# Kernel optimization log

Hardware: AMD Instinct MI355X
Metric: run time of the kernel (lower is better)

Reference implementation:

```python
import jax, jax.numpy as jnp
import numpy as np

B, T1, T2 = 16, 2048, 512
N_MEL, N_TEXT, N_ATT = 80, 256, 256
TEMPERATURE = 0.0005


def _conv1d(x, w, b):
    # x: (B, T, Cin), w: (K, Cin, Cout), 'same' padding
    pad = (w.shape[0] - 1) // 2
    y = jax.lax.conv_general_dilated(
        x, w, window_strides=(1,), padding=[(pad, pad)],
        dimension_numbers=("NWC", "WIO", "NWC"))
    return y + b


def setup_inputs() -> dict:
    key = jax.random.key(0)
    ks = jax.random.split(key, 16)
    s = 0.05
    queries = jax.random.normal(ks[0], (B, N_MEL, T1), jnp.float32)
    keys = jax.random.normal(ks[1], (B, T2, N_TEXT), jnp.float32)
    attn_prior = jax.random.uniform(ks[2], (B, T2, T1), jnp.float32)
    lengths = jax.random.randint(ks[3], (B,), T2 // 2, T2 + 1)
    mask = jnp.arange(T2)[None, :] >= lengths[:, None]  # True = padding
    # key_proj params: Conv(256->512,k3), ReLU, Conv(512->256,k1)
    kw1 = jax.random.normal(ks[4], (3, N_TEXT, 2 * N_TEXT), jnp.float32) * s
    kb1 = jnp.zeros((2 * N_TEXT,), jnp.float32)
    kw2 = jax.random.normal(ks[5], (1, 2 * N_TEXT, N_ATT), jnp.float32) * s
    kb2 = jnp.zeros((N_ATT,), jnp.float32)
    # query_proj params: Conv(80->160,k3), ReLU, Conv(160->80,k1), ReLU, Conv(80->256,k1)
    qw1 = jax.random.normal(ks[6], (3, N_MEL, 2 * N_MEL), jnp.float32) * s
    qb1 = jnp.zeros((2 * N_MEL,), jnp.float32)
    qw2 = jax.random.normal(ks[7], (1, 2 * N_MEL, N_MEL), jnp.float32) * s
    qb2 = jnp.zeros((N_MEL,), jnp.float32)
    qw3 = jax.random.normal(ks[8], (1, N_MEL, N_ATT), jnp.float32) * s
    qb3 = jnp.zeros((N_ATT,), jnp.float32)
    return dict(queries=queries, keys=keys, mask=mask, attn_prior=attn_prior,
                kw1=kw1, kb1=kb1, kw2=kw2, kb2=kb2,
                qw1=qw1, qb1=qb1, qw2=qw2, qb2=qb2, qw3=qw3, qb3=qb3)


def reference(queries, keys, mask, attn_prior,
              kw1, kb1, kw2, kb2, qw1, qb1, qw2, qb2, qw3, qb3):
    # keys: (B, T2, C_text) -> ke: (B, T2, n_att)
    ke = _conv1d(jax.nn.relu(_conv1d(keys, kw1, kb1)), kw2, kb2)
    # queries: (B, C_mel, T1) -> (B, T1, C_mel) -> qe: (B, T1, n_att)
    q = queries.transpose(0, 2, 1)
    q = jax.nn.relu(_conv1d(jax.nn.relu(_conv1d(q, qw1, qb1)), qw2, qb2))
    qe = _conv1d(q, qw3, qb3)
    # pairwise squared L2 distance over channels, via |q|^2 + |k|^2 - 2 q.k
    q2 = jnp.sum(qe * qe, axis=-1)            # (B, T1)
    k2 = jnp.sum(ke * ke, axis=-1)            # (B, T2)
    qk = jnp.einsum("btc,bsc->bts", qe, ke)   # (B, T1, T2)
    dist = q2[:, :, None] + k2[:, None, :] - 2.0 * qk
    attn = (-TEMPERATURE * dist)[:, None]      # (B, 1, T1, T2)
    # prior in log-space
    attn = jax.nn.log_softmax(attn, axis=3) + jnp.log(
        attn_prior.transpose(0, 2, 1)[:, None] + 1e-8)
    attn_logprob = attn
    attn = jnp.where(mask[:, None, None, :], -jnp.inf, attn)
    attn = jax.nn.softmax(attn, axis=3)
    return attn, attn_logprob
```

## Files before the change

### kernel.cpp

```cpp
#include <hip/hip_runtime.h>
#include <cmath>

#define NB    16
#define TT1   2048
#define TT2   512
#define NATT  256
#define TEMP  0.0005f

#define KP_SZ   (NB*514*256)
#define KE_SZ   (NB*512*256)
#define QP_SZ   (NB*2050*80)
#define QE_SZ   (NB*2048*256)
#define W1T_SZ  (512*768)
#define W2T_SZ  (256*512)
#define W3T_SZ  (160*256)
#define W4T_SZ  (80*160)
#define W5T_SZ  (256*96)
#define WTOT_SZ (W1T_SZ+W2T_SZ+W3T_SZ+W4T_SZ+W5T_SZ)
#define LGP_SZ  (NB*TT1*TT2)

#define PREP_PK_BLK   (KP_SZ/256)
#define PREP_WT_BLK   (WTOT_SZ/256)
#define PREP_QT_BLK   (NB*(TT1/64))
#define CONV_KEY_BLK  (NB*512/32)
#define CONV_QRY_BLK  (NB*2048/128)

typedef __attribute__((ext_vector_type(8))) short short8v;
typedef __attribute__((ext_vector_type(4))) float f32x4;

__device__ inline ushort f2bf(float f) {
    unsigned int u = __float_as_uint(f);
    u += 0x7fff + ((u >> 16) & 1);
    return (ushort)(u >> 16);
}
__device__ inline float bf2f(ushort u) {
    return __uint_as_float(((unsigned int)u) << 16);
}


__global__ __launch_bounds__(256) void prep_kernel(
    const float* __restrict__ keys, ushort* __restrict__ kp,
    const float* __restrict__ kw1, const float* __restrict__ kw2,
    const float* __restrict__ qw1, const float* __restrict__ qw2,
    const float* __restrict__ qw3,
    ushort* __restrict__ w1t, ushort* __restrict__ w2t, ushort* __restrict__ w3t,
    ushort* __restrict__ w4t, ushort* __restrict__ w5t,
    const float* __restrict__ queries, ushort* __restrict__ qp)
{
    __shared__ float T[80][65];
    const int bx  = blockIdx.x;
    const int tid = threadIdx.x;

    if (bx < PREP_PK_BLK) {
        const int idx = bx * 256 + tid;
        int c = idx & 255;
        int r = (idx >> 8) % 514;
        int b = idx / (514 * 256);
        float v = 0.f;
        if (r >= 1 && r <= 512)
            v = keys[((size_t)b * 512 + (r - 1)) * 256 + c];
        kp[idx] = f2bf(v);
        return;
    }
    if (bx < PREP_PK_BLK + PREP_WT_BLK) {
        int idx = (bx - PREP_PK_BLK) * 256 + tid;
        const float* w; ushort* wt; int Kreal, Kpad, N;
        if (idx < W1T_SZ) {
            w = kw1; wt = w1t; Kreal = 768; Kpad = 768; N = 512;
        } else if ((idx -= W1T_SZ) < W2T_SZ) {
            w = kw2; wt = w2t; Kreal = 512; Kpad = 512; N = 256;
        } else if ((idx -= W2T_SZ) < W3T_SZ) {
            w = qw1; wt = w3t; Kreal = 240; Kpad = 256; N = 160;
        } else if ((idx -= W3T_SZ) < W4T_SZ) {
            w = qw2; wt = w4t; Kreal = 160; Kpad = 160; N = 80;
        } else {
            idx -= W4T_SZ;
            w = qw3; wt = w5t; Kreal = 80; Kpad = 96; N = 256;
        }
        int k = idx % Kpad;
        int n = idx / Kpad;
        wt[idx] = (k < Kreal) ? f2bf(w[(size_t)k * N + n]) : (ushort)0;
        return;
    }
    {
        const int l  = bx - PREP_PK_BLK - PREP_WT_BLK;
        const int b  = l >> 5;
        const int t0 = (l & 31) * 64;
        const int g  = tid >> 6;
        const int j  = tid & 63;
        #pragma unroll
        for (int r = 0; r < 20; ++r) {
            const int c = g * 20 + r;
            T[c][j] = queries[((size_t)b * 80 + c) * 2048 + t0 + j];
        }
        __syncthreads();
        const int tt = tid >> 2;
        const int c0 = (tid & 3) * 20;
        ushort* qrow = qp + (size_t)b * (2050 * 80) + (size_t)(t0 + tt + 1) * 80 + c0;
        #pragma unroll
        for (int i4 = 0; i4 < 5; ++i4) {
            ushort4 st;
            st.x = f2bf(T[c0 + i4 * 4 + 0][tt]);
            st.y = f2bf(T[c0 + i4 * 4 + 1][tt]);
            st.z = f2bf(T[c0 + i4 * 4 + 2][tt]);
            st.w = f2bf(T[c0 + i4 * 4 + 3][tt]);
            *(ushort4*)(qrow + i4 * 4) = st;
        }
        if (t0 == 0 && tid < 80)
            qp[(size_t)b * (2050 * 80) + tid] = 0;
        if (t0 == 2048 - 64 && tid < 80)
            qp[(size_t)b * (2050 * 80) + (size_t)2049 * 80 + tid] = 0;
    }
}


__global__ __launch_bounds__(512, 4) void conv_kernel(
    const ushort* __restrict__ kp, const ushort* __restrict__ w1t,
    const float* __restrict__ kb1, const ushort* __restrict__ w2t,
    const float* __restrict__ kb2, ushort* __restrict__ ke, float* __restrict__ k2,
    const ushort* __restrict__ qp, const ushort* __restrict__ w3t,
    const float* __restrict__ qb1, const ushort* __restrict__ w4t,
    const float* __restrict__ qb2, const ushort* __restrict__ w5t,
    const float* __restrict__ qb3, ushort* __restrict__ qe)
{
    __shared__ __align__(16) unsigned char smem[69632];
    const int bx   = blockIdx.x;
    const int tid  = threadIdx.x;
    const int wv   = tid >> 6;
    const int lane = tid & 63;
    const int lr   = lane & 15;
    const int lk   = lane >> 4;

    if (bx < CONV_KEY_BLK) {
        ushort (*h1s)[536] = (ushort(*)[536])smem;
        float (*k2part)[8] = (float(*)[8])(smem + 32 * 536 * 2);
        const int m0 = bx * 32;

        {
            const ushort* arow0;
            const ushort* arow1;
            {
                const int m = m0 + lr;
                arow0 = kp + (size_t)(m >> 9) * (514 * 256) + (size_t)(m & 511) * 256 + lk * 8;
                const int m1 = m0 + 16 + lr;
                arow1 = kp + (size_t)(m1 >> 9) * (514 * 256) + (size_t)(m1 & 511) * 256 + lk * 8;
            }
            const ushort* wtb = w1t + (size_t)(wv * 64 + lr) * 768 + lk * 8;
            f32x4 acc[2][4];
            #pragma unroll
            for (int mf = 0; mf < 2; ++mf)
                #pragma unroll
                for (int f = 0; f < 4; ++f) acc[mf][f] = (f32x4){0.f, 0.f, 0.f, 0.f};
            #pragma unroll
            for (int ks = 0; ks < 24; ++ks) {
                const short8v a0 = *(const short8v*)(arow0 + ks * 32);
                const short8v a1 = *(const short8v*)(arow1 + ks * 32);
                #pragma unroll
                for (int f = 0; f < 4; ++f) {
                    const short8v b = *(const short8v*)(wtb + (size_t)f * 16 * 768 + ks * 32);
                    acc[0][f] = __builtin_amdgcn_mfma_f32_16x16x32_bf16(a0, b, acc[0][f], 0, 0, 0);
                    acc[1][f] = __builtin_amdgcn_mfma_f32_16x16x32_bf16(a1, b, acc[1][f], 0, 0, 0);
                }
            }
            #pragma unroll
            for (int f = 0; f < 4; ++f) {
                const int col = wv * 64 + f * 16 + lr;
                const float bv = kb1[col];
                #pragma unroll
                for (int mf = 0; mf < 2; ++mf)
                    #pragma unroll
                    for (int r = 0; r < 4; ++r)
                        h1s[mf * 16 + lk * 4 + r][col] = f2bf(fmaxf(acc[mf][f][r] + bv, 0.f));
            }
        }
        __syncthreads();

        {
            f32x4 acc[2][2];
            #pragma unroll
            for (int mf = 0; mf < 2; ++mf)
                #pragma unroll
                for (int f = 0; f < 2; ++f) acc[mf][f] = (f32x4){0.f, 0.f, 0.f, 0.f};
            #pragma unroll
            for (int ks = 0; ks < 16; ++ks) {
                const short8v a0 = *(const short8v*)&h1s[lr][lk * 8 + ks * 32];
                const short8v a1 = *(const short8v*)&h1s[16 + lr][lk * 8 + ks * 32];
                #pragma unroll
                for (int f = 0; f < 2; ++f) {
                    const short8v b = *(const short8v*)(w2t + (size_t)(wv * 32 + f * 16 + lr) * 512
                                                            + lk * 8 + ks * 32);
                    acc[0][f] = __builtin_amdgcn_mfma_f32_16x16x32_bf16(a0, b, acc[0][f], 0, 0, 0);
                    acc[1][f] = __builtin_amdgcn_mfma_f32_16x16x32_bf16(a1, b, acc[1][f], 0, 0, 0);
                }
            }
            float ss[2][4];
            #pragma unroll
            for (int mf = 0; mf < 2; ++mf)
                #pragma unroll
                for (int r = 0; r < 4; ++r) ss[mf][r] = 0.f;
            #pragma unroll
            for (int f = 0; f < 2; ++f) {
                const int col = wv * 32 + f * 16 + lr;
                const float bv = kb2[col];
                #pragma unroll
                for (int mf = 0; mf < 2; ++mf)
                    #pragma unroll
                    for (int r = 0; r < 4; ++r) {
                        const float o = acc[mf][f][r] + bv;
                        ke[(size_t)(m0 + mf * 16 + lk * 4 + r) * 256 + col] = f2bf(o);
                        ss[mf][r] += o * o;
                    }
            }
            #pragma unroll
            for (int mf = 0; mf < 2; ++mf)
                #pragma unroll
                for (int r = 0; r < 4; ++r) {
                    #pragma unroll
                    for (int off = 1; off < 16; off <<= 1)
                        ss[mf][r] += __shfl_xor(ss[mf][r], off);
                }
            if (lr == 0) {
                #pragma unroll
                for (int mf = 0; mf < 2; ++mf)
                    #pragma unroll
                    for (int r = 0; r < 4; ++r)
                        k2part[mf * 16 + lk * 4 + r][wv] = ss[mf][r];
            }
        }
        __syncthreads();
        if (tid < 32) {
            float s = 0.f;
            #pragma unroll
            for (int w = 0; w < 8; ++w) s += k2part[tid][w];
            k2[m0 + tid] = -TEMP * s;
        }
        return;
    }
    {
        ushort (*s1)[168] = (ushort(*)[168])smem;
        ushort (*s2)[104] = (ushort(*)[104])(smem + 128 * 168 * 2);
        const int m0 = (bx - CONV_KEY_BLK) * 128;
        const int cg = wv >> 2;
        const int rb = (wv & 3) * 32;

        #pragma unroll
        for (int i = 0; i < 4; ++i) {
            const int e = tid * 4 + i;
            s2[e >> 4][80 + (e & 15)] = 0;
        }

        {
            const ushort* arow0;
            const ushort* arow1;
            {
                const int m = m0 + rb + lr;
                arow0 = qp + (size_t)(m >> 11) * (2050 * 80) + (size_t)(m & 2047) * 80 + lk * 8;
                const int m1 = m0 + rb + 16 + lr;
                arow1 = qp + (size_t)(m1 >> 11) * (2050 * 80) + (size_t)(m1 & 2047) * 80 + lk * 8;
            }
            f32x4 acc[2][5];
            #pragma unroll
            for (int mf = 0; mf < 2; ++mf)
                #pragma unroll
                for (int f = 0; f < 5; ++f) acc[mf][f] = (f32x4){0.f, 0.f, 0.f, 0.f};
            #pragma unroll
            for (int ks = 0; ks < 8; ++ks) {
                const short8v a0 = *(const short8v*)(arow0 + ks * 32);
                const short8v a1 = *(const short8v*)(arow1 + ks * 32);
                #pragma unroll
                for (int f = 0; f < 5; ++f) {
                    const short8v b = *(const short8v*)(w3t + (size_t)((cg * 5 + f) * 16 + lr) * 256
                                                            + lk * 8 + ks * 32);
                    acc[0][f] = __builtin_amdgcn_mfma_f32_16x16x32_bf16(a0, b, acc[0][f], 0, 0, 0);
                    acc[1][f] = __builtin_amdgcn_mfma_f32_16x16x32_bf16(a1, b, acc[1][f], 0, 0, 0);
                }
            }
            #pragma unroll
            for (int f = 0; f < 5; ++f) {
                const int col = (cg * 5 + f) * 16 + lr;
                const float bv = qb1[col];
                #pragma unroll
                for (int mf = 0; mf < 2; ++mf)
                    #pragma unroll
                    for (int r = 0; r < 4; ++r)
                        s1[rb + mf * 16 + lk * 4 + r][col] = f2bf(fmaxf(acc[mf][f][r] + bv, 0.f));
            }
        }
        __syncthreads();

        {
            const int nf = cg ? 2 : 3;
            const int f0 = cg ? 3 : 0;
            f32x4 acc[2][3];
            #pragma unroll
            for (int mf = 0; mf < 2; ++mf)
                #pragma unroll
                for (int f = 0; f < 3; ++f) acc[mf][f] = (f32x4){0.f, 0.f, 0.f, 0.f};
            #pragma unroll
            for (int ks = 0; ks < 5; ++ks) {
                const short8v a0 = *(const short8v*)&s1[rb + lr][lk * 8 + ks * 32];
                const short8v a1 = *(const short8v*)&s1[rb + 16 + lr][lk * 8 + ks * 32];
                #pragma unroll
                for (int f = 0; f < 3; ++f) {
                    if (f < nf) {
                        const short8v b = *(const short8v*)(w4t + (size_t)((f0 + f) * 16 + lr) * 160
                                                                + lk * 8 + ks * 32);
                        acc[0][f] = __builtin_amdgcn_mfma_f32_16x16x32_bf16(a0, b, acc[0][f], 0, 0, 0);
                        acc[1][f] = __builtin_amdgcn_mfma_f32_16x16x32_bf16(a1, b, acc[1][f], 0, 0, 0);
                    }
                }
            }
            #pragma unroll
            for (int f = 0; f < 3; ++f) {
                if (f < nf) {
                    const int col = (f0 + f) * 16 + lr;
                    const float bv = qb2[col];
                    #pragma unroll
                    for (int mf = 0; mf < 2; ++mf)
                        #pragma unroll
                        for (int r = 0; r < 4; ++r)
                            s2[rb + mf * 16 + lk * 4 + r][col] = f2bf(fmaxf(acc[mf][f][r] + bv, 0.f));
                }
            }
        }
        __syncthreads();

        {
            f32x4 acc[2][8];
            #pragma unroll
            for (int mf = 0; mf < 2; ++mf)
                #pragma unroll
                for (int f = 0; f < 8; ++f) acc[mf][f] = (f32x4){0.f, 0.f, 0.f, 0.f};
            #pragma unroll
            for (int ks = 0; ks < 3; ++ks) {
                const short8v a0 = *(const short8v*)&s2[rb + lr][lk * 8 + ks * 32];
                const short8v a1 = *(const short8v*)&s2[rb + 16 + lr][lk * 8 + ks * 32];
                #pragma unroll
                for (int f = 0; f < 8; ++f) {
                    const short8v b = *(const short8v*)(w5t + (size_t)((cg * 8 + f) * 16 + lr) * 96
                                                            + lk * 8 + ks * 32);
                    acc[0][f] = __builtin_amdgcn_mfma_f32_16x16x32_bf16(a0, b, acc[0][f], 0, 0, 0);
                    acc[1][f] = __builtin_amdgcn_mfma_f32_16x16x32_bf16(a1, b, acc[1][f], 0, 0, 0);
                }
            }
            #pragma unroll
            for (int f = 0; f < 8; ++f) {
                const int col = (cg * 8 + f) * 16 + lr;
                const float bv = qb3[col];
                #pragma unroll
                for (int mf = 0; mf < 2; ++mf)
                    #pragma unroll
                    for (int r = 0; r < 4; ++r)
                        qe[(size_t)(m0 + rb + mf * 16 + lk * 4 + r) * 256 + col] = f2bf(acc[mf][f][r] + bv);
            }
        }
    }
}


__global__ __launch_bounds__(256) void prior_log_transpose(
    const float* __restrict__ prior, ushort* __restrict__ lgp)
{
    __shared__ float T[64][65];
    const int b    = blockIdx.z;
    const int t1_0 = blockIdx.x * 64;
    const int t2_0 = blockIdx.y * 64;
    const int j  = threadIdx.x & 63;
    const int i0 = (threadIdx.x >> 6) * 16;
    #pragma unroll
    for (int r = 0; r < 16; ++r)
        T[i0 + r][j] = __builtin_nontemporal_load(
            prior + ((size_t)b * TT2 + t2_0 + i0 + r) * TT1 + t1_0 + j);
    __syncthreads();
    #pragma unroll
    for (int r = 0; r < 16; ++r) {
        const int p = i0 + r;
        const float v = T[j][p];
        lgp[((size_t)b * TT1 + t1_0 + p) * TT2 + t2_0 + j] = f2bf(__logf(v + 1e-8f));
    }
}


__global__ __launch_bounds__(512) void attn_kernel(
    const ushort* __restrict__ qe, const ushort* __restrict__ ke,
    const float* __restrict__ k2t, const ushort* __restrict__ lgp,
    const unsigned char* __restrict__ mask,
    float* __restrict__ out_attn, float* __restrict__ out_lp)
{
    __shared__ float S[16][516];
    __shared__ float rowZ[16];
    __shared__ float rowM[16];
    __shared__ float rowI[16];
    const int b    = blockIdx.x >> 7;
    const int t1_0 = (blockIdx.x & 127) << 4;
    const int tid  = threadIdx.x;
    const int lane = tid & 63;
    const int wv   = tid >> 6;
    const int t2   = tid;

    const bool mv = mask[(size_t)b * TT2 + t2] != 0;
    ushort lg[16];
    #pragma unroll
    for (int r = 0; r < 16; ++r)
        lg[r] = lgp[((size_t)b * TT1 + t1_0 + r) * TT2 + t2];

    {
        const int lr = lane & 15;
        const int lk = lane >> 4;
        const ushort* qrow = qe + ((size_t)b * TT1 + t1_0 + lr) * NATT + lk * 8;
        short8v a[8];
        #pragma unroll
        for (int k = 0; k < 8; ++k)
            a[k] = *(const short8v*)(qrow + k * 32);

        const ushort* kbase = ke + ((size_t)b * TT2 + wv * 64 + lr) * NATT + lk * 8;
        #pragma unroll
        for (int n = 0; n < 4; ++n) {
            f32x4 acc = {0.f, 0.f, 0.f, 0.f};
            const ushort* kb = kbase + (size_t)n * 16 * NATT;
            #pragma unroll
            for (int k = 0; k < 8; ++k) {
                short8v bfr = *(const short8v*)(kb + k * 32);
                acc = __builtin_amdgcn_mfma_f32_16x16x32_bf16(a[k], bfr, acc, 0, 0, 0);
            }
            const int col = wv * 64 + n * 16 + lr;
            const float k2v = k2t[(size_t)b * TT2 + col];
            #pragma unroll
            for (int r = 0; r < 4; ++r)
                S[lk * 4 + r][col] = fmaf(2.0f * TEMP, acc[r], k2v);
        }
    }
    __syncthreads();

    const int rr = tid >> 5;
    const int jj = tid & 31;

    {
        float sv[16];
        #pragma unroll
        for (int k = 0; k < 16; ++k) sv[k] = S[rr][jj + 32 * k];
        float mx = sv[0];
        #pragma unroll
        for (int k = 1; k < 16; ++k) mx = fmaxf(mx, sv[k]);
        #pragma unroll
        for (int off = 16; off; off >>= 1) mx = fmaxf(mx, __shfl_xor(mx, off));
        float se = 0.f;
        #pragma unroll
        for (int k = 0; k < 16; ++k) se += __expf(sv[k] - mx);
        #pragma unroll
        for (int off = 16; off; off >>= 1) se += __shfl_xor(se, off);
        if (jj == 0) rowZ[rr] = mx + __logf(se);
    }
    __syncthreads();

    #pragma unroll
    for (int r = 0; r < 16; ++r) {
        const float uu = S[r][t2] + bf2f(lg[r]);
        out_lp[((size_t)b * TT1 + t1_0 + r) * TT2 + t2] = uu - rowZ[r];
        S[r][t2] = mv ? -INFINITY : uu;
    }
    __syncthreads();

    {
        float uv[16];
        #pragma unroll
        for (int k = 0; k < 16; ++k) uv[k] = S[rr][jj + 32 * k];
        float mx = uv[0];
        #pragma unroll
        for (int k = 1; k < 16; ++k) mx = fmaxf(mx, uv[k]);
        #pragma unroll
        for (int off = 16; off; off >>= 1) mx = fmaxf(mx, __shfl_xor(mx, off));
        float se = 0.f;
        #pragma unroll
        for (int k = 0; k < 16; ++k) se += __expf(uv[k] - mx);
        #pragma unroll
        for (int off = 16; off; off >>= 1) se += __shfl_xor(se, off);
        if (jj == 0) { rowM[rr] = mx; rowI[rr] = 1.0f / se; }
    }
    __syncthreads();

    #pragma unroll
    for (int r = 0; r < 16; ++r) {
        const float a = __expf(S[r][t2] - rowM[r]) * rowI[r];
        out_attn[((size_t)b * TT1 + t1_0 + r) * TT2 + t2] = a;
    }
}


extern "C" void kernel_launch(void* const* d_in, const int* in_sizes, int n_in,
                              void* d_out, int out_size, void* d_ws, size_t ws_size,
                              hipStream_t stream) {
    const float* queries = (const float*)d_in[0];
    const float* keys    = (const float*)d_in[1];
    const unsigned char* mask = (const unsigned char*)d_in[2];
    const float* prior   = (const float*)d_in[3];
    const float* kw1 = (const float*)d_in[4];
    const float* kb1 = (const float*)d_in[5];
    const float* kw2 = (const float*)d_in[6];
    const float* kb2 = (const float*)d_in[7];
    const float* qw1 = (const float*)d_in[8];
    const float* qb1 = (const float*)d_in[9];
    const float* qw2 = (const float*)d_in[10];
    const float* qb2 = (const float*)d_in[11];
    const float* qw3 = (const float*)d_in[12];
    const float* qb3 = (const float*)d_in[13];

    ushort* us   = (ushort*)d_ws;
    ushort* kp   = us;
    ushort* ke   = kp  + KP_SZ;
    ushort* qp   = ke  + KE_SZ;
    ushort* qe   = qp  + QP_SZ;
    ushort* w1t  = qe  + QE_SZ;
    ushort* w2t  = w1t + W1T_SZ;
    ushort* w3t  = w2t + W2T_SZ;
    ushort* w4t  = w3t + W3T_SZ;
    ushort* w5t  = w4t + W4T_SZ;
    ushort* lgp  = w5t + W5T_SZ;
    float*  k2   = (float*)(lgp + LGP_SZ);

    float* out_attn = (float*)d_out;
    float* out_lp   = out_attn + (size_t)NB * TT1 * TT2;

    prep_kernel<<<PREP_PK_BLK + PREP_WT_BLK + PREP_QT_BLK, 256, 0, stream>>>(
        keys, kp, kw1, kw2, qw1, qw2, qw3, w1t, w2t, w3t, w4t, w5t, queries, qp);

    conv_kernel<<<CONV_KEY_BLK + CONV_QRY_BLK, 512, 0, stream>>>(
        kp, w1t, kb1, w2t, kb2, ke, k2,
        qp, w3t, qb1, w4t, qb2, w5t, qb3, qe);

    prior_log_transpose<<<dim3(TT1 / 64, TT2 / 64, NB), 256, 0, stream>>>(prior, lgp);

    attn_kernel<<<NB * (TT1 / 16), 512, 0, stream>>>(
        qe, ke, k2, lgp, mask, out_attn, out_lp);
}
```

Measured before the change: 177.4 us.

## Fuse prior log-transpose into conv kernel and restructure attention softmax epilogue

The standalone prior log-transpose kernel is merged into the conv kernel as extra blocks, so it runs concurrently with the key/query projections and saves one launch. In the attention kernel, the output stores are deferred so log-prob and attn are written together from registers, and masked entries are set to zero directly instead of recomputing exp from shared memory. The launch bounds also request 8 waves per SIMD. Risks: more register pressure from holding uu[16], and conv blocks sharing the grid with bandwidth-heavy transpose blocks.

```diff
diff --git a/kernel.cpp b/kernel.cpp
--- a/kernel.cpp
+++ b/kernel.cpp
@@ -24,6 +24,7 @@
 #define PREP_QT_BLK   (NB*(TT1/64))
 #define CONV_KEY_BLK  (NB*512/32)
 #define CONV_QRY_BLK  (NB*2048/128)
+#define CONV_PLT_BLK  (NB*(TT1/64)*(TT2/128))
 
 typedef __attribute__((ext_vector_type(8))) short short8v;
 typedef __attribute__((ext_vector_type(4))) float f32x4;
@@ -114,14 +115,15 @@
 }
 
 
-__global__ __launch_bounds__(512, 4) void conv_kernel(
+__global__ __launch_bounds__(512, 4) void conv_plt_kernel(
     const ushort* __restrict__ kp, const ushort* __restrict__ w1t,
     const float* __restrict__ kb1, const ushort* __restrict__ w2t,
     const float* __restrict__ kb2, ushort* __restrict__ ke, float* __restrict__ k2,
     const ushort* __restrict__ qp, const ushort* __restrict__ w3t,
     const float* __restrict__ qb1, const ushort* __restrict__ w4t,
     const float* __restrict__ qb2, const ushort* __restrict__ w5t,
-    const float* __restrict__ qb3, ushort* __restrict__ qe)
+    const float* __restrict__ qb3, ushort* __restrict__ qe,
+    const float* __restrict__ prior, ushort* __restrict__ lgp)
 {
     __shared__ __align__(16) unsigned char smem[69632];
     const int bx   = blockIdx.x;
@@ -236,7 +238,7 @@
         }
         return;
     }
-    {
+    if (bx < CONV_KEY_BLK + CONV_QRY_BLK) {
         ushort (*s1)[168] = (ushort(*)[168])smem;
         ushort (*s2)[104] = (ushort(*)[104])(smem + 128 * 168 * 2);
         const int m0 = (bx - CONV_KEY_BLK) * 128;
@@ -354,34 +356,34 @@
                         qe[(size_t)(m0 + rb + mf * 16 + lk * 4 + r) * 256 + col] = f2bf(acc[mf][f][r] + bv);
             }
         }
+        return;
+    }
+    {
+        float (*T)[65] = ((float(*)[65])smem) + (size_t)(tid >> 8) * 64;
+        const int l    = bx - CONV_KEY_BLK - CONV_QRY_BLK;
+        const int b    = l >> 7;
+        const int rem  = l & 127;
+        const int t1_0 = (rem & 31) * 64;
+        const int t2_0 = (rem >> 5) * 128 + (tid >> 8) * 64;
+        const int t    = tid & 255;
+        const int j  = t & 63;
+        const int i0 = (t >> 6) * 16;
+        #pragma unroll
+        for (int r = 0; r < 16; ++r)
+            T[i0 + r][j] = __builtin_nontemporal_load(
+                prior + ((size_t)b * TT2 + t2_0 + i0 + r) * TT1 + t1_0 + j);
+        __syncthreads();
+        #pragma unroll
+        for (int r = 0; r < 16; ++r) {
+            const int p = i0 + r;
+            const float v = T[j][p];
+            lgp[((size_t)b * TT1 + t1_0 + p) * TT2 + t2_0 + j] = f2bf(__logf(v + 1e-8f));
+        }
     }
 }
 
 
-__global__ __launch_bounds__(256) void prior_log_transpose(
-    const float* __restrict__ prior, ushort* __restrict__ lgp)
-{
-    __shared__ float T[64][65];
-    const int b    = blockIdx.z;
-    const int t1_0 = blockIdx.x * 64;
-    const int t2_0 = blockIdx.y * 64;
-    const int j  = threadIdx.x & 63;
-    const int i0 = (threadIdx.x >> 6) * 16;
-    #pragma unroll
-    for (int r = 0; r < 16; ++r)
-        T[i0 + r][j] = __builtin_nontemporal_load(
-            prior + ((size_t)b * TT2 + t2_0 + i0 + r) * TT1 + t1_0 + j);
-    __syncthreads();
-    #pragma unroll
-    for (int r = 0; r < 16; ++r) {
-        const int p = i0 + r;
-        const float v = T[j][p];
-        lgp[((size_t)b * TT1 + t1_0 + p) * TT2 + t2_0 + j] = f2bf(__logf(v + 1e-8f));
-    }
-}
-
-
-__global__ __launch_bounds__(512) void attn_kernel(
+__global__ __launch_bounds__(512, 8) void attn_kernel(
     const ushort* __restrict__ qe, const ushort* __restrict__ ke,
     const float* __restrict__ k2t, const ushort* __restrict__ lgp,
     const unsigned char* __restrict__ mask,
@@ -436,53 +438,49 @@
     const int jj = tid & 31;
 
     {
-        float sv[16];
-        #pragma unroll
-        for (int k = 0; k < 16; ++k) sv[k] = S[rr][jj + 32 * k];
-        float mx = sv[0];
-        #pragma unroll
-        for (int k = 1; k < 16; ++k) mx = fmaxf(mx, sv[k]);
+        float mx = -INFINITY;
+        #pragma unroll
+        for (int k = 0; k < 16; ++k) mx = fmaxf(mx, S[rr][jj + 32 * k]);
         #pragma unroll
         for (int off = 16; off; off >>= 1) mx = fmaxf(mx, __shfl_xor(mx, off));
         float se = 0.f;
         #pragma unroll
-        for (int k = 0; k < 16; ++k) se += __expf(sv[k] - mx);
+        for (int k = 0; k < 16; ++k) se += __expf(S[rr][jj + 32 * k] - mx);
         #pragma unroll
         for (int off = 16; off; off >>= 1) se += __shfl_xor(se, off);
         if (jj == 0) rowZ[rr] = mx + __logf(se);
     }
     __syncthreads();
 
+    float uu[16];
     #pragma unroll
     for (int r = 0; r < 16; ++r) {
-        const float uu = S[r][t2] + bf2f(lg[r]);
-        out_lp[((size_t)b * TT1 + t1_0 + r) * TT2 + t2] = uu - rowZ[r];
-        S[r][t2] = mv ? -INFINITY : uu;
+        uu[r] = S[r][t2] + bf2f(lg[r]);
+        S[r][t2] = mv ? -INFINITY : uu[r];
     }
     __syncthreads();
 
     {
-        float uv[16];
-        #pragma unroll
-        for (int k = 0; k < 16; ++k) uv[k] = S[rr][jj + 32 * k];
-        float mx = uv[0];
-        #pragma unroll
-        for (int k = 1; k < 16; ++k) mx = fmaxf(mx, uv[k]);
+        float mx = -INFINITY;
+        #pragma unroll
+        for (int k = 0; k < 16; ++k) mx = fmaxf(mx, S[rr][jj + 32 * k]);
         #pragma unroll
         for (int off = 16; off; off >>= 1) mx = fmaxf(mx, __shfl_xor(mx, off));
         float se = 0.f;
         #pragma unroll
-        for (int k = 0; k < 16; ++k) se += __expf(uv[k] - mx);
+        for (int k = 0; k < 16; ++k) se += __expf(S[rr][jj + 32 * k] - mx);
         #pragma unroll
         for (int off = 16; off; off >>= 1) se += __shfl_xor(se, off);
         if (jj == 0) { rowM[rr] = mx; rowI[rr] = 1.0f / se; }
     }
     __syncthreads();
 
+    float* lpb = out_lp   + ((size_t)b * TT1 + t1_0) * TT2 + t2;
+    float* atb = out_attn + ((size_t)b * TT1 + t1_0) * TT2 + t2;
     #pragma unroll
     for (int r = 0; r < 16; ++r) {
-        const float a = __expf(S[r][t2] - rowM[r]) * rowI[r];
-        out_attn[((size_t)b * TT1 + t1_0 + r) * TT2 + t2] = a;
+        lpb[(size_t)r * TT2] = uu[r] - rowZ[r];
+        atb[(size_t)r * TT2] = mv ? 0.f : __expf(uu[r] - rowM[r]) * rowI[r];
     }
 }
 
@@ -524,11 +522,10 @@
     prep_kernel<<<PREP_PK_BLK + PREP_WT_BLK + PREP_QT_BLK, 256, 0, stream>>>(
         keys, kp, kw1, kw2, qw1, qw2, qw3, w1t, w2t, w3t, w4t, w5t, queries, qp);
 
-    conv_kernel<<<CONV_KEY_BLK + CONV_QRY_BLK, 512, 0, stream>>>(
+    conv_plt_kernel<<<CONV_KEY_BLK + CONV_QRY_BLK + CONV_PLT_BLK, 512, 0, stream>>>(
         kp, w1t, kb1, w2t, kb2, ke, k2,
-        qp, w3t, qb1, w4t, qb2, w5t, qb3, qe);
-
-    prior_log_transpose<<<dim3(TT1 / 64, TT2 / 64, NB), 256, 0, stream>>>(prior, lgp);
+        qp, w3t, qb1, w4t, qb2, w5t, qb3, qe,
+        prior, lgp);
 
     attn_kernel<<<NB * (TT1 / 16), 512, 0, stream>>>(
         qe, ke, k2, lgp, mask, out_attn, out_lp);
```

After: 184.5 us. 4.0% more time.

## Fold prior log-transpose into prep kernel and software-pipeline conv GEMM loads

Applied to the files above, without the earlier changes.

Moves the prior log-transpose work into the prep kernel as extra blocks, which removes one kernel launch and lets that work overlap with the key and weight preparation. It also adds register double-buffering (prefetching the next k-slice) to the MFMA loops of the key conv layers and the first query conv layer. This is meant to hide global-load latency and cut launch overhead, at the cost of more registers and a larger prep grid.

```diff
diff --git a/kernel.cpp b/kernel.cpp
--- a/kernel.cpp
+++ b/kernel.cpp
@@ -19,6 +19,7 @@
 #define WTOT_SZ (W1T_SZ+W2T_SZ+W3T_SZ+W4T_SZ+W5T_SZ)
 #define LGP_SZ  (NB*TT1*TT2)
 
+#define PREP_PLT_BLK  ((TT1/64)*(TT2/64)*NB)
 #define PREP_PK_BLK   (KP_SZ/256)
 #define PREP_WT_BLK   (WTOT_SZ/256)
 #define PREP_QT_BLK   (NB*(TT1/64))
@@ -45,14 +46,35 @@
     const float* __restrict__ qw3,
     ushort* __restrict__ w1t, ushort* __restrict__ w2t, ushort* __restrict__ w3t,
     ushort* __restrict__ w4t, ushort* __restrict__ w5t,
-    const float* __restrict__ queries, ushort* __restrict__ qp)
+    const float* __restrict__ queries, ushort* __restrict__ qp,
+    const float* __restrict__ prior, ushort* __restrict__ lgp)
 {
     __shared__ float T[80][65];
     const int bx  = blockIdx.x;
     const int tid = threadIdx.x;
 
-    if (bx < PREP_PK_BLK) {
-        const int idx = bx * 256 + tid;
+    if (bx < PREP_PLT_BLK) {
+        const int l    = bx;
+        const int t1_0 = (l & 31) * 64;
+        const int t2_0 = ((l >> 5) & 7) * 64;
+        const int b    = l >> 8;
+        const int j  = tid & 63;
+        const int i0 = (tid >> 6) * 16;
+        #pragma unroll
+        for (int r = 0; r < 16; ++r)
+            T[i0 + r][j] = __builtin_nontemporal_load(
+                prior + ((size_t)b * TT2 + t2_0 + i0 + r) * TT1 + t1_0 + j);
+        __syncthreads();
+        #pragma unroll
+        for (int r = 0; r < 16; ++r) {
+            const int p = i0 + r;
+            const float v = T[j][p];
+            lgp[((size_t)b * TT1 + t1_0 + p) * TT2 + t2_0 + j] = f2bf(__logf(v + 1e-8f));
+        }
+        return;
+    }
+    if (bx < PREP_PLT_BLK + PREP_PK_BLK) {
+        const int idx = (bx - PREP_PLT_BLK) * 256 + tid;
         int c = idx & 255;
         int r = (idx >> 8) % 514;
         int b = idx / (514 * 256);
@@ -62,8 +84,8 @@
         kp[idx] = f2bf(v);
         return;
     }
-    if (bx < PREP_PK_BLK + PREP_WT_BLK) {
-        int idx = (bx - PREP_PK_BLK) * 256 + tid;
+    if (bx < PREP_PLT_BLK + PREP_PK_BLK + PREP_WT_BLK) {
+        int idx = (bx - PREP_PLT_BLK - PREP_PK_BLK) * 256 + tid;
         const float* w; ushort* wt; int Kreal, Kpad, N;
         if (idx < W1T_SZ) {
             w = kw1; wt = w1t; Kreal = 768; Kpad = 768; N = 512;
@@ -83,7 +105,7 @@
         return;
     }
     {
-        const int l  = bx - PREP_PK_BLK - PREP_WT_BLK;
+        const int l  = bx - PREP_PLT_BLK - PREP_PK_BLK - PREP_WT_BLK;
         const int b  = l >> 5;
         const int t0 = (l & 31) * 64;
         const int g  = tid >> 6;
@@ -151,17 +173,39 @@
             for (int mf = 0; mf < 2; ++mf)
                 #pragma unroll
                 for (int f = 0; f < 4; ++f) acc[mf][f] = (f32x4){0.f, 0.f, 0.f, 0.f};
+
+            short8v a0 = *(const short8v*)(arow0);
+            short8v a1 = *(const short8v*)(arow1);
+            short8v b0 = *(const short8v*)(wtb);
+            short8v b1 = *(const short8v*)(wtb + (size_t)1 * 16 * 768);
+            short8v b2 = *(const short8v*)(wtb + (size_t)2 * 16 * 768);
+            short8v b3 = *(const short8v*)(wtb + (size_t)3 * 16 * 768);
             #pragma unroll
             for (int ks = 0; ks < 24; ++ks) {
-                const short8v a0 = *(const short8v*)(arow0 + ks * 32);
-                const short8v a1 = *(const short8v*)(arow1 + ks * 32);
-                #pragma unroll
-                for (int f = 0; f < 4; ++f) {
-                    const short8v b = *(const short8v*)(wtb + (size_t)f * 16 * 768 + ks * 32);
-                    acc[0][f] = __builtin_amdgcn_mfma_f32_16x16x32_bf16(a0, b, acc[0][f], 0, 0, 0);
-                    acc[1][f] = __builtin_amdgcn_mfma_f32_16x16x32_bf16(a1, b, acc[1][f], 0, 0, 0);
-                }
-            }
+                short8v na0, na1, nb0, nb1, nb2, nb3;
+                if (ks < 23) {
+                    const int o = (ks + 1) * 32;
+                    na0 = *(const short8v*)(arow0 + o);
+                    na1 = *(const short8v*)(arow1 + o);
+                    nb0 = *(const short8v*)(wtb + o);
+                    nb1 = *(const short8v*)(wtb + (size_t)1 * 16 * 768 + o);
+                    nb2 = *(const short8v*)(wtb + (size_t)2 * 16 * 768 + o);
+                    nb3 = *(const short8v*)(wtb + (size_t)3 * 16 * 768 + o);
+                }
+                acc[0][0] = __builtin_amdgcn_mfma_f32_16x16x32_bf16(a0, b0, acc[0][0], 0, 0, 0);
+                acc[1][0] = __builtin_amdgcn_mfma_f32_16x16x32_bf16(a1, b0, acc[1][0], 0, 0, 0);
+                acc[0][1] = __builtin_amdgcn_mfma_f32_16x16x32_bf16(a0, b1, acc[0][1], 0, 0, 0);
+                acc[1][1] = __builtin_amdgcn_mfma_f32_16x16x32_bf16(a1, b1, acc[1][1], 0, 0, 0);
+                acc[0][2] = __builtin_amdgcn_mfma_f32_16x16x32_bf16(a0, b2, acc[0][2], 0, 0, 0);
+                acc[1][2] = __builtin_amdgcn_mfma_f32_16x16x32_bf16(a1, b2, acc[1][2], 0, 0, 0);
+                acc[0][3] = __builtin_amdgcn_mfma_f32_16x16x32_bf16(a0, b3, acc[0][3], 0, 0, 0);
+                acc[1][3] = __builtin_amdgcn_mfma_f32_16x16x32_bf16(a1, b3, acc[1][3], 0, 0, 0);
+                if (ks < 23) {
+                    a0 = na0; a1 = na1; b0 = nb0; b1 = nb1; b2 = nb2; b3 = nb3;
+                }
+            }
+            const short8v bb[4] = {b0, b1, b2, b3};
+            (void)bb;
             #pragma unroll
             for (int f = 0; f < 4; ++f) {
                 const int col = wv * 64 + f * 16 + lr;
@@ -181,17 +225,24 @@
             for (int mf = 0; mf < 2; ++mf)
                 #pragma unroll
                 for (int f = 0; f < 2; ++f) acc[mf][f] = (f32x4){0.f, 0.f, 0.f, 0.f};
+            const ushort* w2b = w2t + (size_t)(wv * 32 + lr) * 512 + lk * 8;
+            short8v b0 = *(const short8v*)(w2b);
+            short8v b1 = *(const short8v*)(w2b + (size_t)16 * 512);
             #pragma unroll
             for (int ks = 0; ks < 16; ++ks) {
+                short8v nb0, nb1;
+                if (ks < 15) {
+                    const int o = (ks + 1) * 32;
+                    nb0 = *(const short8v*)(w2b + o);
+                    nb1 = *(const short8v*)(w2b + (size_t)16 * 512 + o);
+                }
                 const short8v a0 = *(const short8v*)&h1s[lr][lk * 8 + ks * 32];
                 const short8v a1 = *(const short8v*)&h1s[16 + lr][lk * 8 + ks * 32];
-                #pragma unroll
-                for (int f = 0; f < 2; ++f) {
-                    const short8v b = *(const short8v*)(w2t + (size_t)(wv * 32 + f * 16 + lr) * 512
-                                                            + lk * 8 + ks * 32);
-                    acc[0][f] = __builtin_amdgcn_mfma_f32_16x16x32_bf16(a0, b, acc[0][f], 0, 0, 0);
-                    acc[1][f] = __builtin_amdgcn_mfma_f32_16x16x32_bf16(a1, b, acc[1][f], 0, 0, 0);
-                }
+                acc[0][0] = __builtin_amdgcn_mfma_f32_16x16x32_bf16(a0, b0, acc[0][0], 0, 0, 0);
+                acc[1][0] = __builtin_amdgcn_mfma_f32_16x16x32_bf16(a1, b0, acc[1][0], 0, 0, 0);
+                acc[0][1] = __builtin_amdgcn_mfma_f32_16x16x32_bf16(a0, b1, acc[0][1], 0, 0, 0);
+                acc[1][1] = __builtin_amdgcn_mfma_f32_16x16x32_bf16(a1, b1, acc[1][1], 0, 0, 0);
+                if (ks < 15) { b0 = nb0; b1 = nb1; }
             }
             float ss[2][4];
             #pragma unroll
@@ -258,21 +309,39 @@
                 const int m1 = m0 + rb + 16 + lr;
                 arow1 = qp + (size_t)(m1 >> 11) * (2050 * 80) + (size_t)(m1 & 2047) * 80 + lk * 8;
             }
+            const ushort* w3b = w3t + (size_t)(cg * 5 * 16 + lr) * 256 + lk * 8;
             f32x4 acc[2][5];
             #pragma unroll
             for (int mf = 0; mf < 2; ++mf)
                 #pragma unroll
                 for (int f = 0; f < 5; ++f) acc[mf][f] = (f32x4){0.f, 0.f, 0.f, 0.f};
+
+            short8v a0 = *(const short8v*)(arow0);
+            short8v a1 = *(const short8v*)(arow1);
+            short8v bq[5];
+            #pragma unroll
+            for (int f = 0; f < 5; ++f)
+                bq[f] = *(const short8v*)(w3b + (size_t)f * 16 * 256);
             #pragma unroll
             for (int ks = 0; ks < 8; ++ks) {
-                const short8v a0 = *(const short8v*)(arow0 + ks * 32);
-                const short8v a1 = *(const short8v*)(arow1 + ks * 32);
+                short8v na0, na1, nb[5];
+                if (ks < 7) {
+                    const int o = (ks + 1) * 32;
+                    na0 = *(const short8v*)(arow0 + o);
+                    na1 = *(const short8v*)(arow1 + o);
+                    #pragma unroll
+                    for (int f = 0; f < 5; ++f)
+                        nb[f] = *(const short8v*)(w3b + (size_t)f * 16 * 256 + o);
+                }
                 #pragma unroll
                 for (int f = 0; f < 5; ++f) {
-                    const short8v b = *(const short8v*)(w3t + (size_t)((cg * 5 + f) * 16 + lr) * 256
-                                                            + lk * 8 + ks * 32);
-                    acc[0][f] = __builtin_amdgcn_mfma_f32_16x16x32_bf16(a0, b, acc[0][f], 0, 0, 0);
-                    acc[1][f] = __builtin_amdgcn_mfma_f32_16x16x32_bf16(a1, b, acc[1][f], 0, 0, 0);
+                    acc[0][f] = __builtin_amdgcn_mfma_f32_16x16x32_bf16(a0, bq[f], acc[0][f], 0, 0, 0);
+                    acc[1][f] = __builtin_amdgcn_mfma_f32_16x16x32_bf16(a1, bq[f], acc[1][f], 0, 0, 0);
+                }
+                if (ks < 7) {
+                    a0 = na0; a1 = na1;
+                    #pragma unroll
+                    for (int f = 0; f < 5; ++f) bq[f] = nb[f];
                 }
             }
             #pragma unroll
@@ -354,29 +423,6 @@
                         qe[(size_t)(m0 + rb + mf * 16 + lk * 4 + r) * 256 + col] = f2bf(acc[mf][f][r] + bv);
             }
         }
-    }
-}
-
-
-__global__ __launch_bounds__(256) void prior_log_transpose(
-    const float* __restrict__ prior, ushort* __restrict__ lgp)
-{
-    __shared__ float T[64][65];
-    const int b    = blockIdx.z;
-    const int t1_0 = blockIdx.x * 64;
-    const int t2_0 = blockIdx.y * 64;
-    const int j  = threadIdx.x & 63;
-    const int i0 = (threadIdx.x >> 6) * 16;
-    #pragma unroll
-    for (int r = 0; r < 16; ++r)
-        T[i0 + r][j] = __builtin_nontemporal_load(
-            prior + ((size_t)b * TT2 + t2_0 + i0 + r) * TT1 + t1_0 + j);
-    __syncthreads();
-    #pragma unroll
-    for (int r = 0; r < 16; ++r) {
-        const int p = i0 + r;
-        const float v = T[j][p];
-        lgp[((size_t)b * TT1 + t1_0 + p) * TT2 + t2_0 + j] = f2bf(__logf(v + 1e-8f));
     }
 }
 
@@ -521,15 +567,14 @@
     float* out_attn = (float*)d_out;
     float* out_lp   = out_attn + (size_t)NB * TT1 * TT2;
 
-    prep_kernel<<<PREP_PK_BLK + PREP_WT_BLK + PREP_QT_BLK, 256, 0, stream>>>(
-        keys, kp, kw1, kw2, qw1, qw2, qw3, w1t, w2t, w3t, w4t, w5t, queries, qp);
+    prep_kernel<<<PREP_PLT_BLK + PREP_PK_BLK + PREP_WT_BLK + PREP_QT_BLK, 256, 0, stream>>>(
+        keys, kp, kw1, kw2, qw1, qw2, qw3, w1t, w2t, w3t, w4t, w5t,
+        queries, qp, prior, lgp);
 
     conv_kernel<<<CONV_KEY_BLK + CONV_QRY_BLK, 512, 0, stream>>>(
         kp, w1t, kb1, w2t, kb2, ke, k2,
         qp, w3t, qb1, w4t, qb2, w5t, qb3, qe);
 
-    prior_log_transpose<<<dim3(TT1 / 64, TT2 / 64, NB), 256, 0, stream>>>(prior, lgp);
-
     attn_kernel<<<NB * (TT1 / 16), 512, 0, stream>>>(
         qe, ke, k2, lgp, mask, out_attn, out_lp);
 }
```

After: 172.4 us. -2.8%, faster.
